# Performance work log

Measured on AMD Instinct MI355X. Metric: run time of the kernel, lower is better.

Reference implementation:

```python
import jax, jax.numpy as jnp
import numpy as np

B, T, D, H = 8, 1024, 512, 8
QD, PD, POSD, VD, K = 32, 4, 48, 64, 31
FF = 4 * D
FF1, FF2, FF3, NLA = FF * 3 // 4, FF, FF * 5 // 4, D * 3 // 4


def _swoosh_l(x):
    return jax.nn.softplus(x - 4.0) - 0.08 * x - 0.035


def _swoosh_r(x):
    return jax.nn.softplus(x - 1.0) - 0.08 * x - 0.313261687


def setup_inputs() -> dict:
    key = jax.random.key(0)
    ks = iter(jax.random.split(key, 64))

    def w(shape, fan_in):
        return jax.random.normal(next(ks), shape, jnp.float32) * (fan_in ** -0.5)

    inp = {
        'x': jax.random.normal(next(ks), (B, T, D), jnp.float32),
        'pos_emb': jax.random.normal(next(ks), (2 * T - 1, POSD), jnp.float32),
        'mask': jnp.ones((B, T), bool),
        'attw_q_w': w((D, H * QD), D), 'attw_k_w': w((D, H * QD), D),
        'attw_pq_w': w((D, H * PD), D), 'attw_pos_w': w((POSD, H * PD), POSD),
        'ff1_in_w': w((D, FF1), D), 'ff1_in_b': jnp.zeros(FF1),
        'ff1_out_w': w((FF1, D), FF1), 'ff1_out_b': jnp.zeros(D),
        'nla_w': w((D, NLA * 3), D), 'nla_b': jnp.zeros(NLA * 3),
        'nla_out_w': w((NLA, D), NLA), 'nla_out_b': jnp.zeros(D),
        'sa1_v_w': w((D, H * VD), D), 'sa1_v_b': jnp.zeros(H * VD),
        'sa1_o_w': w((H * VD, D), H * VD), 'sa1_o_b': jnp.zeros(D),
        'conv1_in_w': w((D, 2 * D), D), 'conv1_in_b': jnp.zeros(2 * D),
        'conv1_dw_w': w((D, 1, K), K), 'conv1_dw_b': jnp.zeros(D),
        'conv1_out_w': w((D, D), D), 'conv1_out_b': jnp.zeros(D),
        'ff2_in_w': w((D, FF2), D), 'ff2_in_b': jnp.zeros(FF2),
        'ff2_out_w': w((FF2, D), FF2), 'ff2_out_b': jnp.zeros(D),
        'mid_scale': jax.random.uniform(next(ks), (D,), jnp.float32),
        'sa2_v_w': w((D, H * VD), D), 'sa2_v_b': jnp.zeros(H * VD),
        'sa2_o_w': w((H * VD, D), H * VD), 'sa2_o_b': jnp.zeros(D),
        'conv2_in_w': w((D, 2 * D), D), 'conv2_in_b': jnp.zeros(2 * D),
        'conv2_dw_w': w((D, 1, K), K), 'conv2_dw_b': jnp.zeros(D),
        'conv2_out_w': w((D, D), D), 'conv2_out_b': jnp.zeros(D),
        'ff3_in_w': w((D, FF3), D), 'ff3_in_b': jnp.zeros(FF3),
        'ff3_out_w': w((FF3, D), FF3), 'ff3_out_b': jnp.zeros(D),
        'norm_bias': jnp.zeros(D), 'norm_log_scale': jnp.zeros(()),
        'out_scale': jax.random.uniform(next(ks), (D,), jnp.float32),
    }
    return inp


def _forward(x, pos_emb, attw_q_w, attw_k_w, attw_pq_w, attw_pos_w,
             ff1_in_w, ff1_in_b, ff1_out_w, ff1_out_b,
             nla_w, nla_b, nla_out_w, nla_out_b,
             sa1_v_w, sa1_v_b, sa1_o_w, sa1_o_b,
             conv1_in_w, conv1_in_b, conv1_dw_w, conv1_dw_b, conv1_out_w, conv1_out_b,
             ff2_in_w, ff2_in_b, ff2_out_w, ff2_out_b,
             mid_scale,
             sa2_v_w, sa2_v_b, sa2_o_w, sa2_o_b,
             conv2_in_w, conv2_in_b, conv2_dw_w, conv2_dw_b, conv2_out_w, conv2_out_b,
             ff3_in_w, ff3_in_b, ff3_out_w, ff3_out_b,
             norm_bias, norm_log_scale, out_scale, mask):
    res = x
    # --- relative-pos multi-head attention weights ---
    q = (x @ attw_q_w).reshape(B, T, H, QD).transpose(0, 2, 1, 3)
    k = (x @ attw_k_w).reshape(B, T, H, QD).transpose(0, 2, 1, 3)
    p = (x @ attw_pq_w).reshape(B, T, H, PD).transpose(0, 2, 1, 3)
    content = jnp.einsum('bhtd,bhsd->bhts', q, k) * (QD ** -0.5)
    rel = (pos_emb @ attw_pos_w).reshape(2 * T - 1, H, PD).transpose(1, 0, 2)
    idx = jnp.arange(T)[:, None] - jnp.arange(T)[None, :] + (T - 1)
    relg = rel[:, idx]  # [H, T, T, PD]
    scores = content + jnp.einsum('bhtd,htsd->bhts', p, relg)
    scores = jnp.where(mask[:, None, None, :], scores, -10000.0)
    attn = jax.nn.softmax(scores, axis=-1)
    attn = jnp.where(mask[:, None, :, None], attn, 0.0)

    def mk(y):
        return jnp.where(mask[..., None], y, 0.0)

    def ff(y, wi, bi, wo, bo):
        return _swoosh_l(y @ wi + bi) @ wo + bo

    def sa(y, vw, vb, ow, ob):
        v = (y @ vw + vb).reshape(B, T, H, VD).transpose(0, 2, 1, 3)
        o = jnp.einsum('bhts,bhsd->bhtd', attn, v).transpose(0, 2, 1, 3).reshape(B, T, H * VD)
        return o @ ow + ob

    def conv(y, iw, ib, dw, db, ow, ob):
        u = y @ iw + ib
        a, g = jnp.split(u, 2, axis=-1)
        a = (a * jax.nn.sigmoid(g)).transpose(0, 2, 1)  # [B, D, T]
        a = jnp.where(mask[:, None, :], a, 0.0)
        c = jax.lax.conv_general_dilated(a, dw, (1,), [(K // 2, K // 2)],
                                         dimension_numbers=('NCH', 'OIH', 'NCH'),
                                         feature_group_count=D) + db[None, :, None]
        c = _swoosh_r(c.transpose(0, 2, 1))
        return mk(c @ ow + ob)

    def bypass(r, u, s):
        s = jnp.clip(s, 0.2, 1.0)  # eval/steady regime
        return r + (u - r) * s

    x = mk(x + ff(x, ff1_in_w, ff1_in_b, ff1_out_w, ff1_out_b))
    # non-linear attention (uses head 0)
    a, b, c = jnp.split(x @ nla_w + nla_b, 3, axis=-1)
    att0 = jnp.einsum('bts,bsd->btd', attn[:, 0], jnp.tanh(b) * c)
    x = mk(x + ((a * att0) @ nla_out_w + nla_out_b))
    x = mk(x + sa(x, sa1_v_w, sa1_v_b, sa1_o_w, sa1_o_b))
    x = mk(x + conv(x, conv1_in_w, conv1_in_b, conv1_dw_w, conv1_dw_b, conv1_out_w, conv1_out_b))
    x = mk(x + ff(x, ff2_in_w, ff2_in_b, ff2_out_w, ff2_out_b))
    x = mk(bypass(res, x, mid_scale))
    x = mk(x + sa(x, sa2_v_w, sa2_v_b, sa2_o_w, sa2_o_b))
    x = mk(x + conv(x, conv2_in_w, conv2_in_b, conv2_dw_w, conv2_dw_b, conv2_out_w, conv2_out_b))
    x = mk(x + ff(x, ff3_in_w, ff3_in_b, ff3_out_w, ff3_out_b))
    # BiasNorm
    rms = jnp.sqrt(jnp.mean((x - norm_bias) ** 2, axis=-1, keepdims=True) + 1e-8)
    x = x / rms * jnp.exp(norm_log_scale)
    x = mk(bypass(res, x, out_scale))
    return x


def reference(x, pos_emb, mask, attw_q_w, attw_k_w, attw_pq_w, attw_pos_w,
              ff1_in_w, ff1_in_b, ff1_out_w, ff1_out_b,
              nla_w, nla_b, nla_out_w, nla_out_b,
              sa1_v_w, sa1_v_b, sa1_o_w, sa1_o_b,
              conv1_in_w, conv1_in_b, conv1_dw_w, conv1_dw_b, conv1_out_w, conv1_out_b,
              ff2_in_w, ff2_in_b, ff2_out_w, ff2_out_b,
              mid_scale,
              sa2_v_w, sa2_v_b, sa2_o_w, sa2_o_b,
              conv2_in_w, conv2_in_b, conv2_dw_w, conv2_dw_b, conv2_out_w, conv2_out_b,
              ff3_in_w, ff3_in_b, ff3_out_w, ff3_out_b,
              norm_bias, norm_log_scale, out_scale):
    return _forward(x, pos_emb, attw_q_w, attw_k_w, attw_pq_w, attw_pos_w,
                    ff1_in_w, ff1_in_b, ff1_out_w, ff1_out_b,
                    nla_w, nla_b, nla_out_w, nla_out_b,
                    sa1_v_w, sa1_v_b, sa1_o_w, sa1_o_b,
                    conv1_in_w, conv1_in_b, conv1_dw_w, conv1_dw_b, conv1_out_w, conv1_out_b,
                    ff2_in_w, ff2_in_b, ff2_out_w, ff2_out_b,
                    mid_scale,
                    sa2_v_w, sa2_v_b, sa2_o_w, sa2_o_b,
                    conv2_in_w, conv2_in_b, conv2_dw_w, conv2_dw_b, conv2_out_w, conv2_out_b,
                    ff3_in_w, ff3_in_b, ff3_out_w, ff3_out_b,
                    norm_bias, norm_log_scale, out_scale, mask)
```

## Files before the change

kernel.cpp:

```cpp
#include <hip/hip_runtime.h>
#include <hip/hip_bf16.h>
#include <math.h>

using bf16 = __hip_bfloat16;
using f16 = _Float16;
typedef short s16x8 __attribute__((ext_vector_type(8)));
typedef f16   f16x2 __attribute__((ext_vector_type(2)));
typedef float f32x4 __attribute__((ext_vector_type(4)));
typedef unsigned int u32;
#define DEV __device__ __forceinline__
#define AS1 __attribute__((address_space(1)))
#define AS3 __attribute__((address_space(3)))

constexpr int Bc = 8, Tc = 1024, Dc = 512, Hc = 8;
constexpr int QDc = 32, PDc = 4, POSDc = 48, VDc = 64;
constexpr int Nrow = Bc * Tc;
constexpr int KWc = 31;

DEV float frcp(float x) { return __builtin_amdgcn_rcpf(x); }
DEV float softplus_f(float y) { return fmaxf(y, 0.f) + __logf(1.f + __expf(-fabsf(y))); }
DEV float swoosh_l_f(float x) { return softplus_f(x - 4.f) - 0.08f * x - 0.035f; }
DEV float swoosh_r_f(float x) { return softplus_f(x - 1.f) - 0.08f * x - 0.313261687f; }
DEV float sigmoid_f(float x)  { return frcp(1.f + __expf(-x)); }
DEV float tanh_f(float x) {
  float e = __expf(2.f * fminf(fmaxf(x, -15.f), 15.f));
  return (e - 1.f) * frcp(e + 1.f);
}
DEV float clip_s(float s)     { return fminf(fmaxf(s, 0.2f), 1.0f); }
DEV float to_f(bf16 x)  { return __bfloat162float(x); }
DEV float b2f(short s) { union { u32 u; float f; } z; z.u = (u32)(unsigned short)s << 16; return z.f; }
DEV short f2bb(float v) { bf16 h = __float2bfloat16(v); return *(short*)&h; }
DEV unsigned short f2h(float v) { f16 h = (f16)v; union { f16 x; unsigned short s; } z; z.x = h; return z.s; }
DEV float h2f(unsigned short s) { union { unsigned short s; f16 x; } z; z.s = s; return (float)z.x; }
DEV u32 packbf(float a, float b) {
  return ((u32)(unsigned short)f2bb(b) << 16) | (u32)(unsigned short)f2bb(a);
}
DEV float dot2(u32 a, u32 b, float c) {
#if __has_builtin(__builtin_amdgcn_fdot2)
  union { u32 u; f16x2 v; } x, y; x.u = a; y.u = b;
  return __builtin_amdgcn_fdot2(x.v, y.v, c, false);
#else
  return c + h2f(a & 0xffff) * h2f(b & 0xffff) + h2f(a >> 16) * h2f(b >> 16);
#endif
}

DEV float wave_sum(float v) {
#pragma unroll
  for (int o = 32; o > 0; o >>= 1) v += __shfl_xor(v, o);
  return v;
}

DEV void gload16(const void* g, void* l) {
  __builtin_amdgcn_global_load_lds((const AS1 u32*)g, (AS3 u32*)l, 16, 0, 0);
}

template <int ACT, int WM, int WN, int FM, int FN>
__global__ __launch_bounds__(256) void gemm_mfma(
    const bf16* __restrict__ A, const bf16* __restrict__ B,
    const float* __restrict__ bias, const float* __restrict__ resid,
    float* __restrict__ Cf, bf16* __restrict__ Cb, bf16* __restrict__ Cb2,
    const bf16* __restrict__ auxb, const float* __restrict__ auxf,
    const float* __restrict__ auxf2,
    int M, int N, int K, int lda, int ldb, int ldc,
    long sAz, long sBo, long sBi, long sCo, long sCi, int nh) {
  constexpr int BM = WM * FM * 16, BN = WN * FN * 16;
  constexpr int NP = (ACT == 2) ? 2 : (ACT == 3) ? 3 : 1;
  constexpr int PANOFF = (ACT == 2) ? 512 : 384;
  constexpr int ASZ = BM * 128, BUF = (BM + NP * BN) * 128;
  constexpr int LPS = BM / 32 + NP * (BN / 32);

  int z = blockIdx.z;
  int zo = z / nh, zi = z - zo * nh;
  A += (long)z * sAz;
  B += (long)zo * sBo + (long)zi * sBi;
  long coff = (long)zo * sCo + (long)zi * sCi;

  __shared__ char lds[2 * BUF];

  int tid = threadIdx.x;
  int lane = tid & 63, w = tid >> 6;
  int wm = w / WN, wn = w % WN;

  int gx = gridDim.x;
  int nwg = gx * gridDim.y;
  int flat = blockIdx.y * gx + blockIdx.x;
  if ((nwg & 7) == 0) flat = (flat & 7) * (nwg >> 3) + (flat >> 3);
  int m0 = (flat / gx) * BM, n0 = (flat % gx) * BN;

  int lrow = lane >> 3, lch = lane & 7;
  const bf16* ga = A + (long)(m0 + w * (BM / 4) + lrow) * lda + ((lch ^ lrow) << 3);
  const bf16* gb = B + (long)(n0 + w * (BN / 4) + lrow) * ldb + ((lch ^ lrow) << 3);

  f32x4 acc[NP][FM][FN];
#pragma unroll
  for (int p = 0; p < NP; ++p)
#pragma unroll
    for (int i = 0; i < FM; ++i)
#pragma unroll
      for (int j = 0; j < FN; ++j) acc[p][i][j] = 0.f;

  int nt = K >> 6;
  {
    char* la = lds + w * (BM / 4) * 128;
#pragma unroll
    for (int i = 0; i < BM / 32; ++i) gload16(ga + (long)(i * 8) * lda, la + i * 1024);
#pragma unroll
    for (int p = 0; p < NP; ++p) {
      const bf16* gp = gb + (long)(p * PANOFF) * ldb;
      char* lb = lds + ASZ + p * BN * 128 + w * (BN / 4) * 128;
#pragma unroll
      for (int i = 0; i < BN / 32; ++i) gload16(gp + (long)(i * 8) * ldb, lb + i * 1024);
    }
  }

  for (int t = 0; t < nt; ++t) {
    char* cA = lds + (t & 1) * BUF;
    if (t + 1 < nt) {
      int k0 = (t + 1) << 6;
      char* base = lds + ((t + 1) & 1) * BUF;
      char* la = base + w * (BM / 4) * 128;
#pragma unroll
      for (int i = 0; i < BM / 32; ++i) gload16(ga + (long)(i * 8) * lda + k0, la + i * 1024);
#pragma unroll
      for (int p = 0; p < NP; ++p) {
        const bf16* gp = gb + (long)(p * PANOFF) * ldb;
        char* lb = base + ASZ + p * BN * 128 + w * (BN / 4) * 128;
#pragma unroll
        for (int i = 0; i < BN / 32; ++i) gload16(gp + (long)(i * 8) * ldb + k0, lb + i * 1024);
      }
      asm volatile("s_waitcnt vmcnt(%0)" :: "n"(LPS) : "memory");
    } else {
      asm volatile("s_waitcnt vmcnt(0)" ::: "memory");
    }
    __builtin_amdgcn_s_barrier();
    __builtin_amdgcn_sched_barrier(0);
#pragma unroll
    for (int ks = 0; ks < 2; ++ks) {
      int cg = ks * 4 + (lane >> 4);
      s16x8 af[FM];
#pragma unroll
      for (int f = 0; f < FM; ++f) {
        int row = wm * FM * 16 + f * 16 + (lane & 15);
        af[f] = *(const s16x8*)(cA + row * 128 + ((cg ^ (row & 7)) << 4));
      }
#pragma unroll
      for (int p = 0; p < NP; ++p) {
        char* cB = cA + ASZ + p * BN * 128;
        s16x8 bfr[FN];
#pragma unroll
        for (int f = 0; f < FN; ++f) {
          int row = wn * FN * 16 + f * 16 + (lane & 15);
          bfr[f] = *(const s16x8*)(cB + row * 128 + ((cg ^ (row & 7)) << 4));
        }
#pragma unroll
        for (int fm = 0; fm < FM; ++fm)
#pragma unroll
          for (int fn = 0; fn < FN; ++fn)
            acc[p][fm][fn] = __builtin_amdgcn_mfma_f32_16x16x32_bf16(
                af[fm], bfr[fn], acc[p][fm][fn], 0, 0, 0);
      }
    }
    __builtin_amdgcn_sched_barrier(0);
    __builtin_amdgcn_s_barrier();
  }

  int rbase = m0 + wm * FM * 16 + (lane >> 4) * 4;
  int cbase = n0 + wn * FN * 16 + (lane & 15);
#pragma unroll
  for (int fn = 0; fn < FN; ++fn) {
    int col = cbase + fn * 16;
    if (col >= N) continue;
    float bv = bias ? bias[col] : 0.f;
#pragma unroll
    for (int fm = 0; fm < FM; ++fm) {
#pragma unroll
      for (int r = 0; r < 4; ++r) {
        int row = rbase + fm * 16 + r;
        if (row >= M) continue;
        long ci = coff + (long)row * ldc + col;
        if constexpr (ACT == 2) {
          float va = acc[0][fm][fn][r] + bv;
          float vg = acc[1][fm][fn][r] + bias[col + 512];
          Cb[ci] = __float2bfloat16(va * sigmoid_f(vg));
        } else if constexpr (ACT == 3) {
          float va = acc[0][fm][fn][r] + bv;
          float vb = acc[1][fm][fn][r] + bias[col + 384];
          float vc = acc[2][fm][fn][r] + bias[col + 768];
          Cb2[ci] = __float2bfloat16(va);
          Cb[ci] = __float2bfloat16(tanh_f(vb) * vc);
        } else if constexpr (ACT == 4) {
          Cb[ci] = __float2bfloat16(acc[0][fm][fn][r] * to_f(auxb[ci]));
        } else if constexpr (ACT == 5) {
          float v = acc[0][fm][fn][r] + bv + resid[ci];
          float rv = auxf[ci];
          float o = rv + (v - rv) * clip_s(auxf2[col]);
          Cf[ci] = o;
          Cb[ci] = __float2bfloat16(o);
        } else {
          float v = acc[0][fm][fn][r] + bv;
          if (ACT == 1) v = swoosh_l_f(v);
          if (resid) v += resid[ci];
          if (Cf) Cf[ci] = v;
          if (Cb) Cb[ci] = __float2bfloat16(v);
        }
      }
    }
  }
}

__global__ __launch_bounds__(256) void gemm_tile_f32(
    const float* __restrict__ A, const float* __restrict__ Bm,
    float* __restrict__ Cf, f16* __restrict__ Ch,
    int M, int N, int K, int lda, int ldb, int ldc) {
  __shared__ float As[16][72];
  __shared__ float Bs[16][72];
  int tid = threadIdx.x;
  int tx = tid & 15, ty = tid >> 4;
  int m0 = blockIdx.y * 64, n0 = blockIdx.x * 64;
  int arow = tid >> 2, ak4 = (tid & 3) * 4;
  int bk = tid >> 4, bn4 = (tid & 15) * 4;
  float acc[4][4] = {};
  for (int k0 = 0; k0 < K; k0 += 16) {
    int gm = m0 + arow;
#pragma unroll
    for (int j = 0; j < 4; ++j) {
      int gk = k0 + ak4 + j;
      As[ak4 + j][arow] = (gm < M && gk < K) ? A[(long)gm * lda + gk] : 0.f;
    }
    int gk = k0 + bk;
#pragma unroll
    for (int j = 0; j < 4; ++j) {
      int gn = n0 + bn4 + j;
      Bs[bk][bn4 + j] = (gk < K && gn < N) ? Bm[(long)gk * ldb + gn] : 0.f;
    }
    __syncthreads();
#pragma unroll
    for (int kk = 0; kk < 16; ++kk) {
      float a4[4], b4[4];
#pragma unroll
      for (int i = 0; i < 4; ++i) a4[i] = As[kk][ty * 4 + i];
#pragma unroll
      for (int i = 0; i < 4; ++i) b4[i] = Bs[kk][tx * 4 + i];
#pragma unroll
      for (int i = 0; i < 4; ++i)
#pragma unroll
        for (int j = 0; j < 4; ++j) acc[i][j] += a4[i] * b4[j];
    }
    __syncthreads();
  }
#pragma unroll
  for (int i = 0; i < 4; ++i) {
    int gm = m0 + ty * 4 + i;
    if (gm >= M) continue;
#pragma unroll
    for (int j = 0; j < 4; ++j) {
      int gn = n0 + tx * 4 + j;
      if (gn < N) {
        if (Cf) Cf[(long)gm * ldc + gn] = acc[i][j];
        if (Ch) Ch[(long)gm * ldc + gn] = (f16)acc[i][j];
      }
    }
  }
}

struct TDesc { const float* src; bf16* dst; int K, N, tile0, ntx; float scale; };
struct TBatch { TDesc d[18]; int n; };

__global__ __launch_bounds__(256) void transpose_batch_kernel(TBatch tb) {
  int tile = blockIdx.x;
  int wi = 0;
#pragma unroll 1
  for (int i = 1; i < 18; ++i)
    if (i < tb.n && tb.d[i].tile0 <= tile) wi = i;
  const float* W = tb.d[wi].src;
  bf16* WT = tb.d[wi].dst;
  int K = tb.d[wi].K, N = tb.d[wi].N;
  float sc = tb.d[wi].scale;
  int lt = tile - tb.d[wi].tile0;
  int ntx = tb.d[wi].ntx;
  int bx = (lt % ntx) * 32, by = (lt / ntx) * 32;

  __shared__ float t[32][33];
  int lx = threadIdx.x & 31, ly = threadIdx.x >> 5;
#pragma unroll
  for (int j = 0; j < 4; ++j) {
    int k = by + ly + j * 8, n = bx + lx;
    if (k < K && n < N) t[ly + j * 8][lx] = W[(long)k * N + n];
  }
  __syncthreads();
#pragma unroll
  for (int j = 0; j < 4; ++j) {
    int n = bx + ly + j * 8, k = by + lx;
    if (n < N && k < K) WT[(long)n * K + k] = __float2bfloat16(t[lx][ly + j * 8] * sc);
  }
}

__global__ __launch_bounds__(256) void transpose_bf16_kernel(
    const bf16* __restrict__ src, bf16* __restrict__ dst, int R, int C) {
  __shared__ short t[64][72];
  int bx = blockIdx.x * 64;
  int by = blockIdx.y * 64;
  int tid = threadIdx.x;
  int r = tid >> 3, c8 = tid & 7;
#pragma unroll
  for (int p = 0; p < 2; ++p) {
    s16x8 v = *(const s16x8*)((const short*)src + (long)(bx + p * 32 + r) * C + by + c8 * 8);
#pragma unroll
    for (int j = 0; j < 8; ++j) t[p * 32 + r][c8 * 8 + j] = v[j];
  }
  __syncthreads();
  int j = tid >> 2, q = tid & 3;
  s16x8 o0, o1;
#pragma unroll
  for (int e = 0; e < 8; ++e) o0[e] = t[q * 16 + e][j];
#pragma unroll
  for (int e = 0; e < 8; ++e) o1[e] = t[q * 16 + 8 + e][j];
  short* dp = (short*)dst + (long)(by + j) * R + bx + q * 16;
  *(s16x8*)dp = o0;
  *(s16x8*)(dp + 8) = o1;
}

__global__ void dw_transpose_kernel(const float* __restrict__ dw1, float* __restrict__ o1,
                                    const float* __restrict__ dw2, float* __restrict__ o2) {
  int i = blockIdx.x * 256 + threadIdx.x;
  if (i >= 2 * 512 * KWc) return;
  const float* s = (i < 512 * KWc) ? dw1 : dw2;
  float* o = (i < 512 * KWc) ? o1 : o2;
  int j = (i < 512 * KWc) ? i : i - 512 * KWc;
  int d = j / KWc, kk = j - d * KWc;
  o[kk * 512 + d] = s[j];
}

__global__ void f2b_kernel(const float* __restrict__ in, bf16* __restrict__ out, int nOct) {
  int i = blockIdx.x * 256 + threadIdx.x;
  if (i >= nOct) return;
  float4 a = *(const float4*)(in + (long)i * 8);
  float4 b = *(const float4*)(in + (long)i * 8 + 4);
  s16x8 o;
  o[0] = f2bb(a.x); o[1] = f2bb(a.y); o[2] = f2bb(a.z); o[3] = f2bb(a.w);
  o[4] = f2bb(b.x); o[5] = f2bb(b.y); o[6] = f2bb(b.z); o[7] = f2bb(b.w);
  *(s16x8*)((short*)out + (long)i * 8) = o;
}

__global__ __launch_bounds__(256) void scores_softmax_fused(
    const bf16* __restrict__ qk, const f16* __restrict__ ph,
    const float* __restrict__ rel, bf16* __restrict__ attn) {
  int bh = blockIdx.y;
  int h = bh & (Hc - 1), b = bh >> 3;
  int t0 = blockIdx.x * 16;
  int tid = threadIdx.x, lane = tid & 63, w = tid >> 6;

  __shared__ unsigned short eS[16 * 1024];
  __shared__ u32 rel01[1040], rel23[1040];
  __shared__ u32 pS[16][2];
  __shared__ float lS[16][4];

  for (int i = tid; i < 1039; i += 256) {
    float4 rv = *(const float4*)(rel + (long)(t0 + i) * 32 + h * 4);
    rel01[i] = ((u32)f2h(rv.y) << 16) | f2h(rv.x);
    rel23[i] = ((u32)f2h(rv.w) << 16) | f2h(rv.z);
  }
  if (tid < 16) {
    const u32* pp = (const u32*)(ph + ((long)(b * Tc + t0 + tid)) * 32 + h * 4);
    pS[tid][0] = pp[0]; pS[tid][1] = pp[1];
  }
  __syncthreads();

  s16x8 af = *(const s16x8*)(qk + ((long)(b * Tc + t0 + (lane & 15))) * 512 +
                             h * QDc + (lane >> 4) * 8);
  int g = lane >> 4;
  u32 p01[4], p23[4];
#pragma unroll
  for (int r = 0; r < 4; ++r) { p01[r] = pS[g * 4 + r][0]; p23[r] = pS[g * 4 + r][1]; }
  float sum[4] = {0.f, 0.f, 0.f, 0.f};
  f32x4 zero = {0.f, 0.f, 0.f, 0.f};
  int cols0 = w * 256;
#pragma unroll 4
  for (int tile = 0; tile < 16; ++tile) {
    int s0 = cols0 + tile * 16;
    s16x8 bfr = *(const s16x8*)(qk + ((long)(b * Tc + s0 + (lane & 15))) * 512 +
                                256 + h * QDc + (lane >> 4) * 8);
    f32x4 acc = __builtin_amdgcn_mfma_f32_16x16x32_bf16(af, bfr, zero, 0, 0, 0);
    int scol = s0 + (lane & 15);
    int idx0 = g * 4 - scol + 1023;
#pragma unroll
    for (int r = 0; r < 4; ++r) {
      int idx = idx0 + r;
      float pos = dot2(p23[r], rel23[idx], dot2(p01[r], rel01[idx], 0.f));
      float e = __expf(acc[r] + pos);
      sum[r] += e;
      *(unsigned short*)((char*)eS + (g * 4 + r) * 2048 + ((scol * 2) ^ (g << 5))) =
          (unsigned short)f2bb(e);
    }
  }
#pragma unroll
  for (int o = 1; o < 16; o <<= 1)
#pragma unroll
    for (int r = 0; r < 4; ++r) sum[r] += __shfl_xor(sum[r], o);
  if ((lane & 15) == 0) {
#pragma unroll
    for (int r = 0; r < 4; ++r) lS[g * 4 + r][w] = sum[r];
  }
  __syncthreads();

#pragma unroll
  for (int rr = 0; rr < 4; ++rr) {
    int row = w * 4 + rr;
    float inv = frcp(lS[row][0] + lS[row][1] + lS[row][2] + lS[row][3]);
    int mask = ((row >> 2) & 3) << 5;
    char* rowbase = (char*)eS + row * 2048;
    u32* grow = (u32*)(attn + ((long)bh * Tc + t0 + row) * Tc);
#pragma unroll
    for (int k = 0; k < 8; ++k) {
      u32 ew = *(u32*)(rowbase + (((lane + k * 64) * 4) ^ mask));
      grow[lane + k * 64] = packbf(b2f((short)(ew & 0xffff)) * inv,
                                   b2f((short)(ew >> 16)) * inv);
    }
  }
}

__global__ __launch_bounds__(256) void dwconv_kernel(
    const bf16* __restrict__ a, const float* __restrict__ dwT,
    const float* __restrict__ db, bf16* __restrict__ c) {
  int i = blockIdx.x * 256 + threadIdx.x;
  int oct = i & 63, bt = i >> 6;
  int t = bt & (Tc - 1), b0 = bt - t;
  float acc0 = db[oct * 8 + 0], acc1 = db[oct * 8 + 1], acc2 = db[oct * 8 + 2],
        acc3 = db[oct * 8 + 3], acc4 = db[oct * 8 + 4], acc5 = db[oct * 8 + 5],
        acc6 = db[oct * 8 + 6], acc7 = db[oct * 8 + 7];
#pragma unroll
  for (int kk = 0; kk < KWc; ++kk) {
    int tt = t + kk - (KWc / 2);
    if ((unsigned)tt < (unsigned)Tc) {
      s16x8 av = *(const s16x8*)((const short*)a + ((long)(b0 + tt) << 9) + oct * 8);
      const float* wp = dwT + kk * 512 + oct * 8;
      float4 w0 = *(const float4*)wp, w1 = *(const float4*)(wp + 4);
      acc0 += b2f(av[0]) * w0.x; acc1 += b2f(av[1]) * w0.y;
      acc2 += b2f(av[2]) * w0.z; acc3 += b2f(av[3]) * w0.w;
      acc4 += b2f(av[4]) * w1.x; acc5 += b2f(av[5]) * w1.y;
      acc6 += b2f(av[6]) * w1.z; acc7 += b2f(av[7]) * w1.w;
    }
  }
  s16x8 o;
  o[0] = f2bb(swoosh_r_f(acc0)); o[1] = f2bb(swoosh_r_f(acc1));
  o[2] = f2bb(swoosh_r_f(acc2)); o[3] = f2bb(swoosh_r_f(acc3));
  o[4] = f2bb(swoosh_r_f(acc4)); o[5] = f2bb(swoosh_r_f(acc5));
  o[6] = f2bb(swoosh_r_f(acc6)); o[7] = f2bb(swoosh_r_f(acc7));
  *(s16x8*)((short*)c + (long)bt * 512 + oct * 8) = o;
}

__global__ __launch_bounds__(256) void rmsnorm_bypass_kernel(
    const float* __restrict__ x, const float* __restrict__ x0,
    const float* __restrict__ nb, const float* __restrict__ nls,
    const float* __restrict__ os, float* __restrict__ out) {
  int row = blockIdx.x;
  int tid = threadIdx.x;
  const float* xr = x + (long)row * 512;
  const float* rr = x0 + (long)row * 512;
  float* orow = out + (long)row * 512;
  float v0 = xr[tid], v1 = xr[tid + 256];
  float d0 = v0 - nb[tid], d1 = v1 - nb[tid + 256];
  float ss = d0 * d0 + d1 * d1;
  __shared__ float red[4];
  int lane = tid & 63, wid = tid >> 6;
  ss = wave_sum(ss);
  if (lane == 0) red[wid] = ss;
  __syncthreads();
  ss = red[0] + red[1] + red[2] + red[3];
  float rms = sqrtf(ss * (1.f / 512.f) + 1e-8f);
  float scl = expf(nls[0]) / rms;
  float r0 = rr[tid], s0 = clip_s(os[tid]);
  orow[tid] = r0 + (v0 * scl - r0) * s0;
  float r1 = rr[tid + 256], s1 = clip_s(os[tid + 256]);
  orow[tid + 256] = r1 + (v1 * scl - r1) * s1;
}

static inline int cdiv(int a, int b) { return (a + b - 1) / b; }

template <int ACT, int WM = 2, int WN = 2, int FM = 2, int FN = 2>
static void mfma_launch(hipStream_t st, const bf16* A, const bf16* B, const float* bias,
                        const float* resid, float* Cf, bf16* Cb, bf16* Cb2,
                        const bf16* auxb, const float* auxf, const float* auxf2,
                        int M, int N, int K, int lda, int ldb, int ldc,
                        int Z = 1, int nh = 1, long sAz = 0, long sBo = 0, long sBi = 0,
                        long sCo = 0, long sCi = 0) {
  dim3 grid(cdiv(N, WN * FN * 16), cdiv(M, WM * FM * 16), Z);
  gemm_mfma<ACT, WM, WN, FM, FN><<<grid, dim3(256), 0, st>>>(
      A, B, bias, resid, Cf, Cb, Cb2, auxb, auxf, auxf2, M, N, K, lda, ldb, ldc,
      sAz, sBo, sBi, sCo, sCi, nh);
}
#define MFMA_AV 4, 1, 2, 4

extern "C" void kernel_launch(void* const* d_in, const int* in_sizes, int n_in,
                              void* d_out, int out_size, void* d_ws, size_t ws_size,
                              hipStream_t stream) {
  const float* x0        = (const float*)d_in[0];
  const float* pos_emb   = (const float*)d_in[1];
  const float* Wq        = (const float*)d_in[3];
  const float* Wk        = (const float*)d_in[4];
  const float* Wpq       = (const float*)d_in[5];
  const float* Wpos      = (const float*)d_in[6];
  const float* ff1_in_w  = (const float*)d_in[7];
  const float* ff1_in_b  = (const float*)d_in[8];
  const float* ff1_out_w = (const float*)d_in[9];
  const float* ff1_out_b = (const float*)d_in[10];
  const float* nla_w     = (const float*)d_in[11];
  const float* nla_b     = (const float*)d_in[12];
  const float* nla_out_w = (const float*)d_in[13];
  const float* nla_out_b = (const float*)d_in[14];
  const float* sa1_v_w   = (const float*)d_in[15];
  const float* sa1_v_b   = (const float*)d_in[16];
  const float* sa1_o_w   = (const float*)d_in[17];
  const float* sa1_o_b   = (const float*)d_in[18];
  const float* cv1_in_w  = (const float*)d_in[19];
  const float* cv1_in_b  = (const float*)d_in[20];
  const float* cv1_dw_w  = (const float*)d_in[21];
  const float* cv1_dw_b  = (const float*)d_in[22];
  const float* cv1_out_w = (const float*)d_in[23];
  const float* cv1_out_b = (const float*)d_in[24];
  const float* ff2_in_w  = (const float*)d_in[25];
  const float* ff2_in_b  = (const float*)d_in[26];
  const float* ff2_out_w = (const float*)d_in[27];
  const float* ff2_out_b = (const float*)d_in[28];
  const float* mid_scale = (const float*)d_in[29];
  const float* sa2_v_w   = (const float*)d_in[30];
  const float* sa2_v_b   = (const float*)d_in[31];
  const float* sa2_o_w   = (const float*)d_in[32];
  const float* sa2_o_b   = (const float*)d_in[33];
  const float* cv2_in_w  = (const float*)d_in[34];
  const float* cv2_in_b  = (const float*)d_in[35];
  const float* cv2_dw_w  = (const float*)d_in[36];
  const float* cv2_dw_b  = (const float*)d_in[37];
  const float* cv2_out_w = (const float*)d_in[38];
  const float* cv2_out_b = (const float*)d_in[39];
  const float* ff3_in_w  = (const float*)d_in[40];
  const float* ff3_in_b  = (const float*)d_in[41];
  const float* ff3_out_w = (const float*)d_in[42];
  const float* ff3_out_b = (const float*)d_in[43];
  const float* norm_bias = (const float*)d_in[44];
  const float* nls       = (const float*)d_in[45];
  const float* out_scale = (const float*)d_in[46];
  float* out = (float*)d_out;

  char* wsb = (char*)d_ws;
  size_t off = 0;
  bf16* attn  = (bf16*)(wsb + off); off += (size_t)Bc * Hc * Tc * Tc * 2;
  float* xA   = (float*)(wsb + off); off += (size_t)Nrow * Dc * 4;
  float* xB   = (float*)(wsb + off); off += (size_t)Nrow * Dc * 4;
  bf16*  xb   = (bf16*)(wsb + off);  off += (size_t)Nrow * Dc * 2;
  bf16*  x0b  = (bf16*)(wsb + off);  off += (size_t)Nrow * Dc * 2;
  bf16*  big1b = (bf16*)(wsb + off); off += (size_t)Nrow * 2560 * 2;
  bf16*  big2b = (bf16*)(wsb + off); off += (size_t)Nrow * Dc * 2;
  bf16*  wT    = (bf16*)(wsb + off); off += (size_t)9961472 * 2;
  float* dwT1  = (float*)(wsb + off); off += (size_t)KWc * 512 * 4;
  float* dwT2  = (float*)(wsb + off); off += (size_t)KWc * 512 * 4;
  bf16*  tbcT  = (bf16*)(wsb + off); off += (size_t)384 * Nrow * 2;
  bf16* big3b = big1b + (size_t)Nrow * 2048;
  bf16* vT    = big2b;
  bf16* qk    = big1b;
  bf16* abuf  = big1b;
  f16*  ph    = (f16*)(big1b + (size_t)Nrow * 512);
  float* relb = (float*)(ph + (size_t)Nrow * 32);

  bf16* p_w = wT;
  auto alloc_w = [&](int n, int k) { bf16* r = p_w; p_w += (size_t)n * k; return r; };
  bf16* ff1_in_wT  = alloc_w(1536, 512);
  bf16* ff1_out_wT = alloc_w(512, 1536);
  bf16* nla_wT     = alloc_w(1152, 512);
  bf16* nla_out_wT = alloc_w(512, 384);
  bf16* sa1_v_wT   = alloc_w(512, 512);
  bf16* sa1_o_wT   = alloc_w(512, 512);
  bf16* cv1_in_wT  = alloc_w(1024, 512);
  bf16* cv1_out_wT = alloc_w(512, 512);
  bf16* ff2_in_wT  = alloc_w(2048, 512);
  bf16* ff2_out_wT = alloc_w(512, 2048);
  bf16* sa2_v_wT   = alloc_w(512, 512);
  bf16* sa2_o_wT   = alloc_w(512, 512);
  bf16* cv2_in_wT  = alloc_w(1024, 512);
  bf16* cv2_out_wT = alloc_w(512, 512);
  bf16* ff3_in_wT  = alloc_w(2560, 512);
  bf16* ff3_out_wT = alloc_w(512, 2560);
  bf16* WqkT       = alloc_w(512, 512);

  const int nOctD = Nrow * 64;

  f2b_kernel<<<cdiv(nOctD, 256), 256, 0, stream>>>(x0, x0b, nOctD);
  {
    TBatch tb{};
    auto add = [&](int idx, const float* s, bf16* d, int K, int N, int& t0, float sc) {
      tb.d[idx] = {s, d, K, N, t0, cdiv(N, 32), sc};
      t0 += cdiv(N, 32) * cdiv(K, 32);
    };
    int t0 = 0;
    add(0,  ff1_in_w,  ff1_in_wT,  512, 1536, t0, 1.f);
    add(1,  ff1_out_w, ff1_out_wT, 1536, 512, t0, 1.f);
    add(2,  nla_w,     nla_wT,     512, 1152, t0, 1.f);
    add(3,  nla_out_w, nla_out_wT, 384, 512,  t0, 1.f);
    add(4,  sa1_v_w,   sa1_v_wT,   512, 512,  t0, 1.f);
    add(5,  sa1_o_w,   sa1_o_wT,   512, 512,  t0, 1.f);
    add(6,  cv1_in_w,  cv1_in_wT,  512, 1024, t0, 1.f);
    add(7,  cv1_out_w, cv1_out_wT, 512, 512,  t0, 1.f);
    add(8,  ff2_in_w,  ff2_in_wT,  512, 2048, t0, 1.f);
    add(9,  ff2_out_w, ff2_out_wT, 2048, 512, t0, 1.f);
    add(10, sa2_v_w,   sa2_v_wT,   512, 512,  t0, 1.f);
    add(11, sa2_o_w,   sa2_o_wT,   512, 512,  t0, 1.f);
    add(12, cv2_in_w,  cv2_in_wT,  512, 1024, t0, 1.f);
    add(13, cv2_out_w, cv2_out_wT, 512, 512,  t0, 1.f);
    add(14, ff3_in_w,  ff3_in_wT,  512, 2560, t0, 1.f);
    add(15, ff3_out_w, ff3_out_wT, 2560, 512, t0, 1.f);
    add(16, Wq,        WqkT,       512, 256,  t0, 0.17677669529663687f);
    add(17, Wk,        WqkT + (size_t)256 * 512, 512, 256, t0, 1.f);
    tb.n = 18;
    transpose_batch_kernel<<<t0, 256, 0, stream>>>(tb);
  }
  dw_transpose_kernel<<<cdiv(2 * 512 * KWc, 256), 256, 0, stream>>>(
      cv1_dw_w, dwT1, cv2_dw_w, dwT2);

  gemm_tile_f32<<<dim3(1, cdiv(2 * Tc - 1, 64)), 256, 0, stream>>>(
      pos_emb, Wpos, relb, nullptr, 2 * Tc - 1, 32, POSDc, POSDc, 32, 32);
  gemm_tile_f32<<<dim3(1, cdiv(Nrow, 64)), 256, 0, stream>>>(
      x0, Wpq, nullptr, ph, Nrow, 32, Dc, Dc, 32, 32);
  mfma_launch<0>(stream, x0b, WqkT, nullptr, nullptr, nullptr, qk, nullptr,
                 nullptr, nullptr, nullptr, Nrow, 512, 512, 512, 512, 512);
  scores_softmax_fused<<<dim3(Tc / 16, 64), 256, 0, stream>>>(qk, ph, relb, attn);

  mfma_launch<1>(stream, x0b, ff1_in_wT, ff1_in_b, nullptr, nullptr, big1b, nullptr,
                 nullptr, nullptr, nullptr, Nrow, 1536, 512, 512, 512, 1536);
  mfma_launch<0>(stream, big1b, ff1_out_wT, ff1_out_b, x0, xA, xb, nullptr,
                 nullptr, nullptr, nullptr, Nrow, 512, 1536, 1536, 1536, 512);

  mfma_launch<3>(stream, xb, nla_wT, nla_b, nullptr, nullptr, big2b, abuf,
                 nullptr, nullptr, nullptr, Nrow, 384, 512, 512, 512, 384);
  transpose_bf16_kernel<<<dim3(Nrow / 64, 384 / 64), 256, 0, stream>>>(
      big2b, tbcT, Nrow, 384);
  mfma_launch<4>(stream, attn, tbcT, nullptr, nullptr, nullptr, big3b, nullptr,
                 abuf, nullptr, nullptr, Tc, 384, Tc, Tc, Nrow, 384,
                 Bc, 1, (long)Hc * Tc * Tc, 1024, 0, (long)Tc * 384, 0);
  mfma_launch<0>(stream, big3b, nla_out_wT, nla_out_b, xA, xB, xb, nullptr,
                 nullptr, nullptr, nullptr, Nrow, 512, 384, 384, 384, 512);

  mfma_launch<0>(stream, xb, sa1_v_wT, sa1_v_b, nullptr, nullptr, big3b, nullptr,
                 nullptr, nullptr, nullptr, Nrow, 512, 512, 512, 512, 512);
  transpose_bf16_kernel<<<dim3(Nrow / 64, 8), 256, 0, stream>>>(big3b, vT, Nrow, 512);
  mfma_launch<0, MFMA_AV>(stream, attn, vT, nullptr, nullptr, nullptr, big3b, nullptr,
                          nullptr, nullptr, nullptr, Tc, VDc, Tc, Tc, Nrow, 512,
                          Bc * Hc, Hc, (long)Tc * Tc, Tc, (long)VDc * Nrow,
                          (long)Tc * 512, VDc);
  mfma_launch<0>(stream, big3b, sa1_o_wT, sa1_o_b, xB, xA, xb, nullptr,
                 nullptr, nullptr, nullptr, Nrow, 512, 512, 512, 512, 512);

  mfma_launch<2>(stream, xb, cv1_in_wT, cv1_in_b, nullptr, nullptr, big2b, nullptr,
                 nullptr, nullptr, nullptr, Nrow, 512, 512, 512, 512, 512);
  dwconv_kernel<<<cdiv(nOctD, 256), 256, 0, stream>>>(big2b, dwT1, cv1_dw_b, big3b);
  mfma_launch<0>(stream, big3b, cv1_out_wT, cv1_out_b, xA, xB, xb, nullptr,
                 nullptr, nullptr, nullptr, Nrow, 512, 512, 512, 512, 512);

  mfma_launch<1>(stream, xb, ff2_in_wT, ff2_in_b, nullptr, nullptr, big1b, nullptr,
                 nullptr, nullptr, nullptr, Nrow, 2048, 512, 512, 512, 2048);
  mfma_launch<5>(stream, big1b, ff2_out_wT, ff2_out_b, xB, xB, xb, nullptr,
                 nullptr, x0, mid_scale, Nrow, 512, 2048, 2048, 2048, 512);

  mfma_launch<0>(stream, xb, sa2_v_wT, sa2_v_b, nullptr, nullptr, big3b, nullptr,
                 nullptr, nullptr, nullptr, Nrow, 512, 512, 512, 512, 512);
  transpose_bf16_kernel<<<dim3(Nrow / 64, 8), 256, 0, stream>>>(big3b, vT, Nrow, 512);
  mfma_launch<0, MFMA_AV>(stream, attn, vT, nullptr, nullptr, nullptr, big3b, nullptr,
                          nullptr, nullptr, nullptr, Tc, VDc, Tc, Tc, Nrow, 512,
                          Bc * Hc, Hc, (long)Tc * Tc, Tc, (long)VDc * Nrow,
                          (long)Tc * 512, VDc);
  mfma_launch<0>(stream, big3b, sa2_o_wT, sa2_o_b, xB, xA, xb, nullptr,
                 nullptr, nullptr, nullptr, Nrow, 512, 512, 512, 512, 512);

  mfma_launch<2>(stream, xb, cv2_in_wT, cv2_in_b, nullptr, nullptr, big2b, nullptr,
                 nullptr, nullptr, nullptr, Nrow, 512, 512, 512, 512, 512);
  dwconv_kernel<<<cdiv(nOctD, 256), 256, 0, stream>>>(big2b, dwT2, cv2_dw_b, big3b);
  mfma_launch<0>(stream, big3b, cv2_out_wT, cv2_out_b, xA, xB, xb, nullptr,
                 nullptr, nullptr, nullptr, Nrow, 512, 512, 512, 512, 512);

  mfma_launch<1>(stream, xb, ff3_in_wT, ff3_in_b, nullptr, nullptr, big1b, nullptr,
                 nullptr, nullptr, nullptr, Nrow, 2560, 512, 512, 512, 2560);
  mfma_launch<0>(stream, big1b, ff3_out_wT, ff3_out_b, xB, xA, nullptr, nullptr,
                 nullptr, nullptr, nullptr, Nrow, 512, 2560, 2560, 2560, 512);

  rmsnorm_bypass_kernel<<<Nrow, 256, 0, stream>>>(xA, x0, norm_bias, nls, out_scale, out);
}
```

Baseline: 767.6 us.

## Fuse QK with FF1-in GEMM, emit transposed V/NLA outputs directly, merge small GEMMs

The QK projection and the FF1 input projection are merged into one GEMM over a concatenated weight (ACT 9), with the epilogue splitting the columns into raw qk and the swoosh-activated FF1 hidden. The NLA and value projections are computed as weight-times-activation GEMMs (ACT 8 and 7), so they write their outputs already transposed, and the separate transpose kernels are removed. The NLA variant now loads three A panels instead of three B panels, and the ACT 4 epilogue reads the gating buffer in transposed layout. The two small fp32 positional GEMMs become a single launch. The aim is fewer launches and less intermediate traffic, at the cost of more complex, hard-coded epilogue indexing.

```diff
diff --git a/kernel.cpp b/kernel.cpp
--- a/kernel.cpp
+++ b/kernel.cpp
@@ -64,10 +64,12 @@
     int M, int N, int K, int lda, int ldb, int ldc,
     long sAz, long sBo, long sBi, long sCo, long sCi, int nh) {
   constexpr int BM = WM * FM * 16, BN = WN * FN * 16;
-  constexpr int NP = (ACT == 2) ? 2 : (ACT == 3) ? 3 : 1;
-  constexpr int PANOFF = (ACT == 2) ? 512 : 384;
-  constexpr int ASZ = BM * 128, BUF = (BM + NP * BN) * 128;
-  constexpr int LPS = BM / 32 + NP * (BN / 32);
+  constexpr int NPA = (ACT == 8) ? 3 : 1;
+  constexpr int NPB = (ACT == 2) ? 2 : 1;
+  constexpr int PANA = 384, PANB = 512;
+  constexpr int ASZT = NPA * BM * 128;
+  constexpr int BUF = (NPA * BM + NPB * BN) * 128;
+  constexpr int LPS = NPA * (BM / 32) + NPB * (BN / 32);
 
   int z = blockIdx.z;
   int zo = z / nh, zi = z - zo * nh;
@@ -91,9 +93,9 @@
   const bf16* ga = A + (long)(m0 + w * (BM / 4) + lrow) * lda + ((lch ^ lrow) << 3);
   const bf16* gb = B + (long)(n0 + w * (BN / 4) + lrow) * ldb + ((lch ^ lrow) << 3);
 
-  f32x4 acc[NP][FM][FN];
-#pragma unroll
-  for (int p = 0; p < NP; ++p)
+  f32x4 acc[NPA * NPB][FM][FN];
+#pragma unroll
+  for (int p = 0; p < NPA * NPB; ++p)
 #pragma unroll
     for (int i = 0; i < FM; ++i)
 #pragma unroll
@@ -101,13 +103,17 @@
 
   int nt = K >> 6;
   {
-    char* la = lds + w * (BM / 4) * 128;
-#pragma unroll
-    for (int i = 0; i < BM / 32; ++i) gload16(ga + (long)(i * 8) * lda, la + i * 1024);
-#pragma unroll
-    for (int p = 0; p < NP; ++p) {
-      const bf16* gp = gb + (long)(p * PANOFF) * ldb;
-      char* lb = lds + ASZ + p * BN * 128 + w * (BN / 4) * 128;
+#pragma unroll
+    for (int pa = 0; pa < NPA; ++pa) {
+      const bf16* gp = ga + (long)(pa * PANA) * lda;
+      char* la = lds + pa * BM * 128 + w * (BM / 4) * 128;
+#pragma unroll
+      for (int i = 0; i < BM / 32; ++i) gload16(gp + (long)(i * 8) * lda, la + i * 1024);
+    }
+#pragma unroll
+    for (int pb = 0; pb < NPB; ++pb) {
+      const bf16* gp = gb + (long)(pb * PANB) * ldb;
+      char* lb = lds + ASZT + pb * BN * 128 + w * (BN / 4) * 128;
 #pragma unroll
       for (int i = 0; i < BN / 32; ++i) gload16(gp + (long)(i * 8) * ldb, lb + i * 1024);
     }
@@ -118,15 +124,19 @@
     if (t + 1 < nt) {
       int k0 = (t + 1) << 6;
       char* base = lds + ((t + 1) & 1) * BUF;
-      char* la = base + w * (BM / 4) * 128;
-#pragma unroll
-      for (int i = 0; i < BM / 32; ++i) gload16(ga + (long)(i * 8) * lda + k0, la + i * 1024);
-#pragma unroll
-      for (int p = 0; p < NP; ++p) {
-        const bf16* gp = gb + (long)(p * PANOFF) * ldb;
-        char* lb = base + ASZ + p * BN * 128 + w * (BN / 4) * 128;
-#pragma unroll
-        for (int i = 0; i < BN / 32; ++i) gload16(gp + (long)(i * 8) * ldb + k0, lb + i * 1024);
+#pragma unroll
+      for (int pa = 0; pa < NPA; ++pa) {
+        const bf16* gp = ga + (long)(pa * PANA) * lda + k0;
+        char* la = base + pa * BM * 128 + w * (BM / 4) * 128;
+#pragma unroll
+        for (int i = 0; i < BM / 32; ++i) gload16(gp + (long)(i * 8) * lda, la + i * 1024);
+      }
+#pragma unroll
+      for (int pb = 0; pb < NPB; ++pb) {
+        const bf16* gp = gb + (long)(pb * PANB) * ldb + k0;
+        char* lb = base + ASZT + pb * BN * 128 + w * (BN / 4) * 128;
+#pragma unroll
+        for (int i = 0; i < BN / 32; ++i) gload16(gp + (long)(i * 8) * ldb, lb + i * 1024);
       }
       asm volatile("s_waitcnt vmcnt(%0)" :: "n"(LPS) : "memory");
     } else {
@@ -137,28 +147,33 @@
 #pragma unroll
     for (int ks = 0; ks < 2; ++ks) {
       int cg = ks * 4 + (lane >> 4);
-      s16x8 af[FM];
-#pragma unroll
-      for (int f = 0; f < FM; ++f) {
-        int row = wm * FM * 16 + f * 16 + (lane & 15);
-        af[f] = *(const s16x8*)(cA + row * 128 + ((cg ^ (row & 7)) << 4));
-      }
-#pragma unroll
-      for (int p = 0; p < NP; ++p) {
-        char* cB = cA + ASZ + p * BN * 128;
-        s16x8 bfr[FN];
+      s16x8 af[NPA][FM], bfr[NPB][FN];
+#pragma unroll
+      for (int pa = 0; pa < NPA; ++pa)
+#pragma unroll
+        for (int f = 0; f < FM; ++f) {
+          int row = wm * FM * 16 + f * 16 + (lane & 15);
+          af[pa][f] = *(const s16x8*)(cA + pa * BM * 128 + row * 128 +
+                                      ((cg ^ (row & 7)) << 4));
+        }
+#pragma unroll
+      for (int pb = 0; pb < NPB; ++pb)
 #pragma unroll
         for (int f = 0; f < FN; ++f) {
           int row = wn * FN * 16 + f * 16 + (lane & 15);
-          bfr[f] = *(const s16x8*)(cB + row * 128 + ((cg ^ (row & 7)) << 4));
+          bfr[pb][f] = *(const s16x8*)(cA + ASZT + pb * BN * 128 + row * 128 +
+                                       ((cg ^ (row & 7)) << 4));
         }
 #pragma unroll
-        for (int fm = 0; fm < FM; ++fm)
-#pragma unroll
-          for (int fn = 0; fn < FN; ++fn)
-            acc[p][fm][fn] = __builtin_amdgcn_mfma_f32_16x16x32_bf16(
-                af[fm], bfr[fn], acc[p][fm][fn], 0, 0, 0);
-      }
+      for (int pa = 0; pa < NPA; ++pa)
+#pragma unroll
+        for (int pb = 0; pb < NPB; ++pb)
+#pragma unroll
+          for (int fm = 0; fm < FM; ++fm)
+#pragma unroll
+            for (int fn = 0; fn < FN; ++fn)
+              acc[pa * NPB + pb][fm][fn] = __builtin_amdgcn_mfma_f32_16x16x32_bf16(
+                  af[pa][fm], bfr[pb][fn], acc[pa * NPB + pb][fm][fn], 0, 0, 0);
     }
     __builtin_amdgcn_sched_barrier(0);
     __builtin_amdgcn_s_barrier();
@@ -170,7 +185,6 @@
   for (int fn = 0; fn < FN; ++fn) {
     int col = cbase + fn * 16;
     if (col >= N) continue;
-    float bv = bias ? bias[col] : 0.f;
 #pragma unroll
     for (int fm = 0; fm < FM; ++fm) {
 #pragma unroll
@@ -179,25 +193,36 @@
         if (row >= M) continue;
         long ci = coff + (long)row * ldc + col;
         if constexpr (ACT == 2) {
-          float va = acc[0][fm][fn][r] + bv;
+          float va = acc[0][fm][fn][r] + bias[col];
           float vg = acc[1][fm][fn][r] + bias[col + 512];
           Cb[ci] = __float2bfloat16(va * sigmoid_f(vg));
-        } else if constexpr (ACT == 3) {
-          float va = acc[0][fm][fn][r] + bv;
-          float vb = acc[1][fm][fn][r] + bias[col + 384];
-          float vc = acc[2][fm][fn][r] + bias[col + 768];
-          Cb2[ci] = __float2bfloat16(va);
-          Cb[ci] = __float2bfloat16(tanh_f(vb) * vc);
         } else if constexpr (ACT == 4) {
-          Cb[ci] = __float2bfloat16(acc[0][fm][fn][r] * to_f(auxb[ci]));
+          float a = to_f(auxb[(long)col * 8192 + (long)zo * 1024 + row]);
+          Cb[ci] = __float2bfloat16(acc[0][fm][fn][r] * a);
         } else if constexpr (ACT == 5) {
-          float v = acc[0][fm][fn][r] + bv + resid[ci];
+          float v = acc[0][fm][fn][r] + bias[col] + resid[ci];
           float rv = auxf[ci];
           float o = rv + (v - rv) * clip_s(auxf2[col]);
           Cf[ci] = o;
           Cb[ci] = __float2bfloat16(o);
+        } else if constexpr (ACT == 7) {
+          Cb[ci] = __float2bfloat16(acc[0][fm][fn][r] + bias[row]);
+        } else if constexpr (ACT == 8) {
+          float va = acc[0][fm][fn][r] + bias[row];
+          float vb = acc[1][fm][fn][r] + bias[row + 384];
+          float vc = acc[2][fm][fn][r] + bias[row + 768];
+          Cb2[ci] = __float2bfloat16(va);
+          Cb[ci] = __float2bfloat16(tanh_f(vb) * vc);
+        } else if constexpr (ACT == 9) {
+          float v = acc[0][fm][fn][r];
+          if (col < 512) {
+            Cb2[(long)row * 512 + col] = __float2bfloat16(v);
+          } else {
+            Cb[(long)row * ldc + (col - 512)] =
+                __float2bfloat16(swoosh_l_f(v + bias[col - 512]));
+          }
         } else {
-          float v = acc[0][fm][fn][r] + bv;
+          float v = acc[0][fm][fn][r] + (bias ? bias[col] : 0.f);
           if (ACT == 1) v = swoosh_l_f(v);
           if (resid) v += resid[ci];
           if (Cf) Cf[ci] = v;
@@ -208,15 +233,24 @@
   }
 }
 
-__global__ __launch_bounds__(256) void gemm_tile_f32(
-    const float* __restrict__ A, const float* __restrict__ Bm,
-    float* __restrict__ Cf, f16* __restrict__ Ch,
-    int M, int N, int K, int lda, int ldb, int ldc) {
+__global__ __launch_bounds__(256) void relph_kernel(
+    const float* __restrict__ pos_emb, const float* __restrict__ Wpos,
+    float* __restrict__ relb,
+    const float* __restrict__ x0, const float* __restrict__ Wpq,
+    f16* __restrict__ ph) {
+  int zz = blockIdx.z;
+  const float* A  = zz ? x0 : pos_emb;
+  const float* Bm = zz ? Wpq : Wpos;
+  int M = zz ? Nrow : (2 * Tc - 1);
+  int K = zz ? Dc : POSDc;
+  int lda = K;
+  int m0 = blockIdx.y * 64;
+  if (m0 >= M) return;
+
   __shared__ float As[16][72];
   __shared__ float Bs[16][72];
   int tid = threadIdx.x;
   int tx = tid & 15, ty = tid >> 4;
-  int m0 = blockIdx.y * 64, n0 = blockIdx.x * 64;
   int arow = tid >> 2, ak4 = (tid & 3) * 4;
   int bk = tid >> 4, bn4 = (tid & 15) * 4;
   float acc[4][4] = {};
@@ -230,8 +264,8 @@
     int gk = k0 + bk;
 #pragma unroll
     for (int j = 0; j < 4; ++j) {
-      int gn = n0 + bn4 + j;
-      Bs[bk][bn4 + j] = (gk < K && gn < N) ? Bm[(long)gk * ldb + gn] : 0.f;
+      int gn = bn4 + j;
+      Bs[bk][bn4 + j] = (gk < K && gn < 32) ? Bm[(long)gk * 32 + gn] : 0.f;
     }
     __syncthreads();
 #pragma unroll
@@ -254,10 +288,10 @@
     if (gm >= M) continue;
 #pragma unroll
     for (int j = 0; j < 4; ++j) {
-      int gn = n0 + tx * 4 + j;
-      if (gn < N) {
-        if (Cf) Cf[(long)gm * ldc + gn] = acc[i][j];
-        if (Ch) Ch[(long)gm * ldc + gn] = (f16)acc[i][j];
+      int gn = tx * 4 + j;
+      if (gn < 32) {
+        if (zz) ph[(long)gm * 32 + gn] = (f16)acc[i][j];
+        else    relb[(long)gm * 32 + gn] = acc[i][j];
       }
     }
   }
@@ -293,31 +327,6 @@
     int n = bx + ly + j * 8, k = by + lx;
     if (n < N && k < K) WT[(long)n * K + k] = __float2bfloat16(t[lx][ly + j * 8] * sc);
   }
-}
-
-__global__ __launch_bounds__(256) void transpose_bf16_kernel(
-    const bf16* __restrict__ src, bf16* __restrict__ dst, int R, int C) {
-  __shared__ short t[64][72];
-  int bx = blockIdx.x * 64;
-  int by = blockIdx.y * 64;
-  int tid = threadIdx.x;
-  int r = tid >> 3, c8 = tid & 7;
-#pragma unroll
-  for (int p = 0; p < 2; ++p) {
-    s16x8 v = *(const s16x8*)((const short*)src + (long)(bx + p * 32 + r) * C + by + c8 * 8);
-#pragma unroll
-    for (int j = 0; j < 8; ++j) t[p * 32 + r][c8 * 8 + j] = v[j];
-  }
-  __syncthreads();
-  int j = tid >> 2, q = tid & 3;
-  s16x8 o0, o1;
-#pragma unroll
-  for (int e = 0; e < 8; ++e) o0[e] = t[q * 16 + e][j];
-#pragma unroll
-  for (int e = 0; e < 8; ++e) o1[e] = t[q * 16 + 8 + e][j];
-  short* dp = (short*)dst + (long)(by + j) * R + bx + q * 16;
-  *(s16x8*)dp = o0;
-  *(s16x8*)(dp + 8) = o1;
 }
 
 __global__ void dw_transpose_kernel(const float* __restrict__ dw1, float* __restrict__ o1,
@@ -557,14 +566,14 @@
   bf16*  tbcT  = (bf16*)(wsb + off); off += (size_t)384 * Nrow * 2;
   bf16* big3b = big1b + (size_t)Nrow * 2048;
   bf16* vT    = big2b;
-  bf16* qk    = big1b;
-  bf16* abuf  = big1b;
-  f16*  ph    = (f16*)(big1b + (size_t)Nrow * 512);
+  bf16* qkb   = big2b;
+  bf16* aT    = big1b;
+  f16*  ph    = (f16*)(big1b + (size_t)Nrow * 1536);
   float* relb = (float*)(ph + (size_t)Nrow * 32);
 
   bf16* p_w = wT;
   auto alloc_w = [&](int n, int k) { bf16* r = p_w; p_w += (size_t)n * k; return r; };
-  bf16* ff1_in_wT  = alloc_w(1536, 512);
+  bf16* qkff1_wT   = alloc_w(2048, 512);
   bf16* ff1_out_wT = alloc_w(512, 1536);
   bf16* nla_wT     = alloc_w(1152, 512);
   bf16* nla_out_wT = alloc_w(512, 384);
@@ -580,7 +589,6 @@
   bf16* cv2_out_wT = alloc_w(512, 512);
   bf16* ff3_in_wT  = alloc_w(2560, 512);
   bf16* ff3_out_wT = alloc_w(512, 2560);
-  bf16* WqkT       = alloc_w(512, 512);
 
   const int nOctD = Nrow * 64;
 
@@ -592,56 +600,48 @@
       t0 += cdiv(N, 32) * cdiv(K, 32);
     };
     int t0 = 0;
-    add(0,  ff1_in_w,  ff1_in_wT,  512, 1536, t0, 1.f);
-    add(1,  ff1_out_w, ff1_out_wT, 1536, 512, t0, 1.f);
-    add(2,  nla_w,     nla_wT,     512, 1152, t0, 1.f);
-    add(3,  nla_out_w, nla_out_wT, 384, 512,  t0, 1.f);
-    add(4,  sa1_v_w,   sa1_v_wT,   512, 512,  t0, 1.f);
-    add(5,  sa1_o_w,   sa1_o_wT,   512, 512,  t0, 1.f);
-    add(6,  cv1_in_w,  cv1_in_wT,  512, 1024, t0, 1.f);
-    add(7,  cv1_out_w, cv1_out_wT, 512, 512,  t0, 1.f);
-    add(8,  ff2_in_w,  ff2_in_wT,  512, 2048, t0, 1.f);
-    add(9,  ff2_out_w, ff2_out_wT, 2048, 512, t0, 1.f);
-    add(10, sa2_v_w,   sa2_v_wT,   512, 512,  t0, 1.f);
-    add(11, sa2_o_w,   sa2_o_wT,   512, 512,  t0, 1.f);
-    add(12, cv2_in_w,  cv2_in_wT,  512, 1024, t0, 1.f);
-    add(13, cv2_out_w, cv2_out_wT, 512, 512,  t0, 1.f);
-    add(14, ff3_in_w,  ff3_in_wT,  512, 2560, t0, 1.f);
-    add(15, ff3_out_w, ff3_out_wT, 2560, 512, t0, 1.f);
-    add(16, Wq,        WqkT,       512, 256,  t0, 0.17677669529663687f);
-    add(17, Wk,        WqkT + (size_t)256 * 512, 512, 256, t0, 1.f);
+    add(0,  Wq,        qkff1_wT,   512, 256,  t0, 0.17677669529663687f);
+    add(1,  Wk,        qkff1_wT + (size_t)256 * 512, 512, 256, t0, 1.f);
+    add(2,  ff1_in_w,  qkff1_wT + (size_t)512 * 512, 512, 1536, t0, 1.f);
+    add(3,  ff1_out_w, ff1_out_wT, 1536, 512, t0, 1.f);
+    add(4,  nla_w,     nla_wT,     512, 1152, t0, 1.f);
+    add(5,  nla_out_w, nla_out_wT, 384, 512,  t0, 1.f);
+    add(6,  sa1_v_w,   sa1_v_wT,   512, 512,  t0, 1.f);
+    add(7,  sa1_o_w,   sa1_o_wT,   512, 512,  t0, 1.f);
+    add(8,  cv1_in_w,  cv1_in_wT,  512, 1024, t0, 1.f);
+    add(9,  cv1_out_w, cv1_out_wT, 512, 512,  t0, 1.f);
+    add(10, ff2_in_w,  ff2_in_wT,  512, 2048, t0, 1.f);
+    add(11, ff2_out_w, ff2_out_wT, 2048, 512, t0, 1.f);
+    add(12, sa2_v_w,   sa2_v_wT,   512, 512,  t0, 1.f);
+    add(13, sa2_o_w,   sa2_o_wT,   512, 512,  t0, 1.f);
+    add(14, cv2_in_w,  cv2_in_wT,  512, 1024, t0, 1.f);
+    add(15, cv2_out_w, cv2_out_wT, 512, 512,  t0, 1.f);
+    add(16, ff3_in_w,  ff3_in_wT,  512, 2560, t0, 1.f);
+    add(17, ff3_out_w, ff3_out_wT, 2560, 512, t0, 1.f);
     tb.n = 18;
     transpose_batch_kernel<<<t0, 256, 0, stream>>>(tb);
   }
   dw_transpose_kernel<<<cdiv(2 * 512 * KWc, 256), 256, 0, stream>>>(
       cv1_dw_w, dwT1, cv2_dw_w, dwT2);
-
-  gemm_tile_f32<<<dim3(1, cdiv(2 * Tc - 1, 64)), 256, 0, stream>>>(
-      pos_emb, Wpos, relb, nullptr, 2 * Tc - 1, 32, POSDc, POSDc, 32, 32);
-  gemm_tile_f32<<<dim3(1, cdiv(Nrow, 64)), 256, 0, stream>>>(
-      x0, Wpq, nullptr, ph, Nrow, 32, Dc, Dc, 32, 32);
-  mfma_launch<0>(stream, x0b, WqkT, nullptr, nullptr, nullptr, qk, nullptr,
-                 nullptr, nullptr, nullptr, Nrow, 512, 512, 512, 512, 512);
-  scores_softmax_fused<<<dim3(Tc / 16, 64), 256, 0, stream>>>(qk, ph, relb, attn);
-
-  mfma_launch<1>(stream, x0b, ff1_in_wT, ff1_in_b, nullptr, nullptr, big1b, nullptr,
-                 nullptr, nullptr, nullptr, Nrow, 1536, 512, 512, 512, 1536);
+  relph_kernel<<<dim3(1, 128, 2), 256, 0, stream>>>(pos_emb, Wpos, relb, x0, Wpq, ph);
+
+  mfma_launch<9>(stream, x0b, qkff1_wT, ff1_in_b, nullptr, nullptr, big1b, qkb,
+                 nullptr, nullptr, nullptr, Nrow, 2048, 512, 512, 512, 1536);
+  scores_softmax_fused<<<dim3(Tc / 16, 64), 256, 0, stream>>>(qkb, ph, relb, attn);
+
   mfma_launch<0>(stream, big1b, ff1_out_wT, ff1_out_b, x0, xA, xb, nullptr,
                  nullptr, nullptr, nullptr, Nrow, 512, 1536, 1536, 1536, 512);
 
-  mfma_launch<3>(stream, xb, nla_wT, nla_b, nullptr, nullptr, big2b, abuf,
-                 nullptr, nullptr, nullptr, Nrow, 384, 512, 512, 512, 384);
-  transpose_bf16_kernel<<<dim3(Nrow / 64, 384 / 64), 256, 0, stream>>>(
-      big2b, tbcT, Nrow, 384);
+  mfma_launch<8>(stream, nla_wT, xb, nla_b, nullptr, nullptr, tbcT, aT,
+                 nullptr, nullptr, nullptr, 384, Nrow, 512, 512, 512, Nrow);
   mfma_launch<4>(stream, attn, tbcT, nullptr, nullptr, nullptr, big3b, nullptr,
-                 abuf, nullptr, nullptr, Tc, 384, Tc, Tc, Nrow, 384,
+                 aT, nullptr, nullptr, Tc, 384, Tc, Tc, Nrow, 384,
                  Bc, 1, (long)Hc * Tc * Tc, 1024, 0, (long)Tc * 384, 0);
   mfma_launch<0>(stream, big3b, nla_out_wT, nla_out_b, xA, xB, xb, nullptr,
                  nullptr, nullptr, nullptr, Nrow, 512, 384, 384, 384, 512);
 
-  mfma_launch<0>(stream, xb, sa1_v_wT, sa1_v_b, nullptr, nullptr, big3b, nullptr,
-                 nullptr, nullptr, nullptr, Nrow, 512, 512, 512, 512, 512);
-  transpose_bf16_kernel<<<dim3(Nrow / 64, 8), 256, 0, stream>>>(big3b, vT, Nrow, 512);
+  mfma_launch<7>(stream, sa1_v_wT, xb, sa1_v_b, nullptr, nullptr, vT, nullptr,
+                 nullptr, nullptr, nullptr, 512, Nrow, 512, 512, 512, Nrow);
   mfma_launch<0, MFMA_AV>(stream, attn, vT, nullptr, nullptr, nullptr, big3b, nullptr,
                           nullptr, nullptr, nullptr, Tc, VDc, Tc, Tc, Nrow, 512,
                           Bc * Hc, Hc, (long)Tc * Tc, Tc, (long)VDc * Nrow,
@@ -660,9 +660,8 @@
   mfma_launch<5>(stream, big1b, ff2_out_wT, ff2_out_b, xB, xB, xb, nullptr,
                  nullptr, x0, mid_scale, Nrow, 512, 2048, 2048, 2048, 512);
 
-  mfma_launch<0>(stream, xb, sa2_v_wT, sa2_v_b, nullptr, nullptr, big3b, nullptr,
-                 nullptr, nullptr, nullptr, Nrow, 512, 512, 512, 512, 512);
-  transpose_bf16_kernel<<<dim3(Nrow / 64, 8), 256, 0, stream>>>(big3b, vT, Nrow, 512);
+  mfma_launch<7>(stream, sa2_v_wT, xb, sa2_v_b, nullptr, nullptr, vT, nullptr,
+                 nullptr, nullptr, nullptr, 512, Nrow, 512, 512, 512, Nrow);
   mfma_launch<0, MFMA_AV>(stream, attn, vT, nullptr, nullptr, nullptr, big3b, nullptr,
                           nullptr, nullptr, nullptr, Tc, VDc, Tc, Tc, Nrow, 512,
                           Bc * Hc, Hc, (long)Tc * Tc, Tc, (long)VDc * Nrow,
```

Measured after the change: 770.8 us. Within noise of the previous version (+0.4%).
